# Kernel optimization log

Measured on AMD Instinct MI355X. Metric: run time of the kernel, lower is better.

## Reference

```python
import jax, jax.numpy as jnp
import numpy as np

IN, H, OUT = 128, 256, 128
B, T = 256, 512
EPS = 1e-5


def gru_cell(x, h, w_ih, w_hh, b_ih, b_hh):
    # PyTorch GRUCell: gates ordered (r, z, n)
    gi = x @ w_ih.T + b_ih            # (B, 3H)
    gh = h @ w_hh.T + b_hh            # (B, 3H)
    gi_r, gi_z, gi_n = jnp.split(gi, 3, axis=-1)
    gh_r, gh_z, gh_n = jnp.split(gh, 3, axis=-1)
    r = jax.nn.sigmoid(gi_r + gh_r)
    z = jax.nn.sigmoid(gi_z + gh_z)
    n = jnp.tanh(gi_n + r * gh_n)
    return (1.0 - z) * n + z * h


def setup_inputs() -> dict:
    key = jax.random.key(0)
    ks = jax.random.split(key, 12)
    s_in = 1.0 / np.sqrt(H)
    u = lambda k, shp: jax.random.uniform(k, shp, jnp.float32, -s_in, s_in)
    return {
        "x": jax.random.normal(ks[0], (B, T, IN), jnp.float32),
        "w_ih1": u(ks[1], (3 * H, IN)),
        "w_hh1": u(ks[2], (3 * H, H)),
        "b_ih1": u(ks[3], (3 * H,)),
        "b_hh1": u(ks[4], (3 * H,)),
        "w_ih2": u(ks[5], (3 * H, H)),
        "w_hh2": u(ks[6], (3 * H, H)),
        "b_ih2": u(ks[7], (3 * H,)),
        "b_hh2": u(ks[8], (3 * H,)),
        "gamma": jnp.ones((H,), jnp.float32),
        "beta": jnp.zeros((H,), jnp.float32),
        "fc_w": u(ks[9], (OUT, H)),
        "fc_b": u(ks[10], (OUT,)),
    }


def reference(x, w_ih1, w_hh1, b_ih1, b_hh1, w_ih2, w_hh2, b_ih2, b_hh2,
              gamma, beta, fc_w, fc_b):
    batch = x.shape[0]
    h0 = (jnp.zeros((batch, H), x.dtype), jnp.zeros((batch, H), x.dtype))

    def step(carry, xt):
        h1, h2 = carry
        h1 = gru_cell(xt, h1, w_ih1, w_hh1, b_ih1, b_hh1)
        h2 = gru_cell(h1, h2, w_ih2, w_hh2, b_ih2, b_hh2)
        return (h1, h2), h2

    _, seq_hidden = jax.lax.scan(step, h0, jnp.swapaxes(x, 0, 1))  # (T, B, H)
    seq_hidden = jnp.swapaxes(seq_hidden, 0, 1)                    # (B, T, H)

    # SyncBatchNorm in training mode: batch statistics over (batch*time)
    flat = seq_hidden.reshape(-1, H)
    mean = flat.mean(axis=0)
    var = flat.var(axis=0)  # biased variance, as used for normalization
    normed = (flat - mean) * jax.lax.rsqrt(var + EPS) * gamma + beta

    # Hardtanh(-2, 2), temporal mean, linear projection
    act = jnp.clip(normed, -2.0, 2.0).reshape(batch, -1, H)
    summary = act.mean(axis=1)                                     # (B, H)
    return summary @ fc_w.T + fc_b
```

## Files before the change

### kernel.cpp

```cpp
#include <hip/hip_runtime.h>
#include <stdint.h>

#define TT 512
#define BB 256
#define HH 256
#define II 128
#define OUTD 128
#define EPSV 1e-5f

#define NCL 32
#define RPC 8
#define RD1 32
#define RD2 16
#define HPAD 264
#define SPIN_CAP (1 << 17)

#define P_M1 0
#define P_A  1
#define P_M2 2
#define P_B  3

#define OFF_PROG     0u
#define OFF_BNSUM    1024u
#define OFF_BNSQ     2048u
#define OFF_ZERO_END 3072u
#define OFF_GI1      65536u
#define GI_SLOT      16384u
#define GI1_BYTES    ((unsigned)NCL*RD1*GI_SLOT)
#define OFF_H1R      (OFF_GI1 + GI1_BYTES)
#define H1R_BYTES    ((unsigned)NCL*RD2*4096u)
#define OFF_GI2      (OFF_H1R + H1R_BYTES)
#define GI2_BYTES    ((unsigned)NCL*RD2*GI_SLOT)
#define OFF_H2SEQ    (OFF_GI2 + GI2_BYTES)

typedef short bf16x8 __attribute__((ext_vector_type(8)));
typedef float f32x4  __attribute__((ext_vector_type(4)));
typedef unsigned long long u64;

__device__ __forceinline__ short f2bf(float v) {
    unsigned u = __float_as_uint(v);
    u += 0x7fffu + ((u >> 16) & 1u);
    return (short)(u >> 16);
}
__device__ __forceinline__ float bf2f(short s) {
    return __uint_as_float(((unsigned)(unsigned short)s) << 16);
}
__device__ __forceinline__ float bf2f_lo(unsigned u) {
    return __uint_as_float(u << 16);
}
__device__ __forceinline__ float bf2f_hi(unsigned u) {
    return __uint_as_float(u & 0xffff0000u);
}
__device__ __forceinline__ unsigned pk2bf(float a, float b) {
    return (unsigned)(unsigned short)f2bf(a) | ((unsigned)(unsigned short)f2bf(b) << 16);
}
__device__ __forceinline__ bf16x8 ldfrag_f32(const float* __restrict__ p) {
    const float4* q = (const float4*)p;
    float4 a = q[0], b = q[1];
    bf16x8 f;
    f[0]=f2bf(a.x); f[1]=f2bf(a.y); f[2]=f2bf(a.z); f[3]=f2bf(a.w);
    f[4]=f2bf(b.x); f[5]=f2bf(b.y); f[6]=f2bf(b.z); f[7]=f2bf(b.w);
    return f;
}
__device__ __forceinline__ float sigm_f(float x) {
    float e = __expf(-x);
    return __builtin_amdgcn_rcpf(1.f + e);
}
__device__ __forceinline__ float tanh_f(float x) {
    float ax = fabsf(x);
    float e  = __expf(-2.f * ax);
    float t  = (1.f - e) * __builtin_amdgcn_rcpf(1.f + e);
    return copysignf(t, x);
}
__device__ __forceinline__ void poll_ge(const unsigned* p, int tgt) {
    if (tgt <= 0) return;
    int spins = 0;
    while ((int)__hip_atomic_load((unsigned*)p, __ATOMIC_RELAXED, __HIP_MEMORY_SCOPE_SYSTEM) < tgt) {
        __builtin_amdgcn_s_sleep(2);
        if (++spins > SPIN_CAP) break;
    }
    asm volatile("" ::: "memory");
}
__device__ __forceinline__ void poll2_ge(const unsigned* p1, int t1, const unsigned* p2, int t2) {
    int spins = 0;
    for (;;) {
        int a = (int)__hip_atomic_load((unsigned*)p1, __ATOMIC_RELAXED, __HIP_MEMORY_SCOPE_SYSTEM);
        int b = (int)__hip_atomic_load((unsigned*)p2, __ATOMIC_RELAXED, __HIP_MEMORY_SCOPE_SYSTEM);
        if (a >= t1 && b >= t2) break;
        __builtin_amdgcn_s_sleep(2);
        if (++spins > SPIN_CAP) break;
    }
    asm volatile("" ::: "memory");
}
__device__ __forceinline__ void post_prog(unsigned* p, int v) {
    __hip_atomic_store(p, (unsigned)v, __ATOMIC_RELAXED, __HIP_MEMORY_SCOPE_SYSTEM);
}
__device__ __forceinline__ unsigned ld_u32_coh(const unsigned* p) {
    return __hip_atomic_load((unsigned*)p, __ATOMIC_RELAXED, __HIP_MEMORY_SCOPE_SYSTEM);
}
__device__ __forceinline__ void st_u32_coh(unsigned* p, unsigned v) {
    __hip_atomic_store(p, v, __ATOMIC_RELAXED, __HIP_MEMORY_SCOPE_SYSTEM);
}
__device__ __forceinline__ u64 ld_u64_coh(const u64* p) {
    return __hip_atomic_load((u64*)p, __ATOMIC_RELAXED, __HIP_MEMORY_SCOPE_SYSTEM);
}
__device__ __forceinline__ void st_u64_coh(u64* p, u64 v) {
    __hip_atomic_store(p, v, __ATOMIC_RELAXED, __HIP_MEMORY_SCOPE_SYSTEM);
}
#define CFENCE() asm volatile("" ::: "memory")

__global__ void __launch_bounds__(512, 1)
gru_pipe(const float* __restrict__ x,
         const float* __restrict__ wih1, const float* __restrict__ whh1,
         const float* __restrict__ bih1, const float* __restrict__ bhh1,
         const float* __restrict__ wih2, const float* __restrict__ whh2,
         const float* __restrict__ bih2, const float* __restrict__ bhh2,
         char* __restrict__ ws)
{
    const int tid = threadIdx.x, wave = tid >> 6, lane = tid & 63;
    const int qd = lane >> 4, ln = lane & 15;
    const int stage = blockIdx.x & 3;
    const int cl    = blockIdx.x >> 2;
    const int grow0 = cl * RPC;

    unsigned* prog = (unsigned*)(ws + OFF_PROG) + cl * 4;
    short* h2seq = (short*)(ws + OFF_H2SEQ);

    __shared__ __align__(16) short hb[2][16][HPAD];
    {
        short* z = &hb[0][0][0];
        for (int i = tid; i < 2*16*HPAD; i += 512) z[i] = 0;
    }
    __syncthreads();

    if (stage == 0) {
        bf16x8 Wi[2][3][4]; f32x4 cinit[2][3];
        #pragma unroll
        for (int b2 = 0; b2 < 2; ++b2)
        #pragma unroll
        for (int g = 0; g < 3; ++g) {
            const int grow = g*256 + (wave*2 + b2)*16 + ln;
            #pragma unroll
            for (int kc = 0; kc < 4; ++kc)
                Wi[b2][g][kc] = ldfrag_f32(wih1 + grow*II + kc*32 + qd*8);
            float c0 = bih1[grow] + (g < 2 ? bhh1[grow] : 0.f);
            cinit[b2][g] = f32x4{c0, c0, c0, c0};
        }
        const float* xr = x + (size_t)(grow0 + (ln>>2)*2 + (ln&1)) * (TT*II) + qd*8;
        float4 xp[8];
        #pragma unroll
        for (int kc = 0; kc < 4; ++kc) {
            xp[2*kc]   = *(const float4*)(xr + kc*32);
            xp[2*kc+1] = *(const float4*)(xr + kc*32 + 4);
        }

        for (int t = 0; t < TT; ++t) {
            if (tid == 0 && t >= 2) post_prog(&prog[P_M1], t);
            if ((t & 7) == 0) poll_ge(&prog[P_A], t - 24);
            CFENCE();
            bf16x8 a[4];
            #pragma unroll
            for (int kc = 0; kc < 4; ++kc) {
                float4 u = xp[2*kc], v = xp[2*kc+1];
                bf16x8 f;
                f[0]=f2bf(u.x); f[1]=f2bf(u.y); f[2]=f2bf(u.z); f[3]=f2bf(u.w);
                f[4]=f2bf(v.x); f[5]=f2bf(v.y); f[6]=f2bf(v.z); f[7]=f2bf(v.w);
                a[kc] = f;
            }
            if (t + 1 < TT) {
                const float* xn = xr + (size_t)(t+1)*II;
                #pragma unroll
                for (int kc = 0; kc < 4; ++kc) {
                    xp[2*kc]   = *(const float4*)(xn + kc*32);
                    xp[2*kc+1] = *(const float4*)(xn + kc*32 + 4);
                }
            }
            CFENCE();
            f32x4 acc[2][3];
            #pragma unroll
            for (int b2 = 0; b2 < 2; ++b2)
            #pragma unroll
            for (int g = 0; g < 3; ++g) acc[b2][g] = cinit[b2][g];
            #pragma unroll
            for (int kc = 0; kc < 4; ++kc)
            #pragma unroll
            for (int b2 = 0; b2 < 2; ++b2)
            #pragma unroll
            for (int g = 0; g < 3; ++g)
                acc[b2][g] = __builtin_amdgcn_mfma_f32_16x16x32_bf16(a[kc], Wi[b2][g][kc], acc[b2][g], 0, 0, 0);
            CFENCE();
            char* slot = ws + OFF_GI1 + ((size_t)cl*RD1 + (t & (RD1-1)))*GI_SLOT;
            unsigned* rz = (unsigned*)slot;
            u64* nn = (u64*)(slot + 8192);
            #pragma unroll
            for (int b2 = 0; b2 < 2; ++b2) {
                const int tile = wave*2 + b2;
                st_u32_coh(rz + (tile*2 + 0)*64 + lane, pk2bf(acc[b2][0][0], acc[b2][0][1]));
                st_u32_coh(rz + (tile*2 + 1)*64 + lane, pk2bf(acc[b2][1][0], acc[b2][1][1]));
                union { float f[2]; u64 u; } np;
                np.f[0] = acc[b2][2][0]; np.f[1] = acc[b2][2][1];
                st_u64_coh(nn + tile*64 + lane, np.u);
            }
            asm volatile("s_waitcnt vmcnt(14)" ::: "memory");
            __builtin_amdgcn_sched_barrier(0);
            __builtin_amdgcn_s_barrier();
        }
        __syncthreads();
        if (tid == 0) post_prog(&prog[P_M1], 1000000);

    } else if (stage == 1) {
        bf16x8 Wh[2][3][8]; float bnn[2];
        #pragma unroll
        for (int b2 = 0; b2 < 2; ++b2) {
            const int colg = (wave*2 + b2)*16 + ln;
            #pragma unroll
            for (int g = 0; g < 3; ++g)
                #pragma unroll
                for (int kc = 0; kc < 8; ++kc)
                    Wh[b2][g][kc] = ldfrag_f32(whh1 + (g*256 + colg)*HH + kc*32 + qd*8);
            bnn[b2] = bhh1[512 + colg];
        }
        float hold[2][2] = {{0.f,0.f},{0.f,0.f}};
        unsigned pr0, pr1, pz0, pz1; u64 pn0, pn1;
        const int tile0 = wave*2, tile1 = wave*2 + 1;

        poll_ge(&prog[P_M1], 2);
        {
            char* slot = ws + OFF_GI1 + (size_t)cl*RD1*GI_SLOT;
            const unsigned* rz = (const unsigned*)slot;
            const u64* nn = (const u64*)(slot + 8192);
            pr0 = ld_u32_coh(rz + (tile0*2+0)*64 + lane);
            pz0 = ld_u32_coh(rz + (tile0*2+1)*64 + lane);
            pn0 = ld_u64_coh(nn + tile0*64 + lane);
            pr1 = ld_u32_coh(rz + (tile1*2+0)*64 + lane);
            pz1 = ld_u32_coh(rz + (tile1*2+1)*64 + lane);
            pn1 = ld_u64_coh(nn + tile1*64 + lane);
        }

        for (int t = 0; t < TT; ++t) {
            if (tid == 0 && t >= 2) post_prog(&prog[P_A], t);
            if ((t & 7) == 0) poll2_ge(&prog[P_M1], t + 10, &prog[P_M2], t - 9);
            CFENCE();
            f32x4 aR[2], aZ[2], aN[2]; float gn[2][2];
            aR[0] = f32x4{bf2f_lo(pr0), bf2f_hi(pr0), 0.f, 0.f};
            aZ[0] = f32x4{bf2f_lo(pz0), bf2f_hi(pz0), 0.f, 0.f};
            aR[1] = f32x4{bf2f_lo(pr1), bf2f_hi(pr1), 0.f, 0.f};
            aZ[1] = f32x4{bf2f_lo(pz1), bf2f_hi(pz1), 0.f, 0.f};
            { union { u64 u; float f[2]; } c; c.u = pn0; gn[0][0]=c.f[0]; gn[0][1]=c.f[1];
              c.u = pn1; gn[1][0]=c.f[0]; gn[1][1]=c.f[1]; }
            aN[0] = f32x4{bnn[0], bnn[0], 0.f, 0.f};
            aN[1] = f32x4{bnn[1], bnn[1], 0.f, 0.f};
            if (t + 1 < TT) {
                char* slot = ws + OFF_GI1 + ((size_t)cl*RD1 + ((t+1) & (RD1-1)))*GI_SLOT;
                const unsigned* rz = (const unsigned*)slot;
                const u64* nn = (const u64*)(slot + 8192);
                pr0 = ld_u32_coh(rz + (tile0*2+0)*64 + lane);
                pz0 = ld_u32_coh(rz + (tile0*2+1)*64 + lane);
                pn0 = ld_u64_coh(nn + tile0*64 + lane);
                pr1 = ld_u32_coh(rz + (tile1*2+0)*64 + lane);
                pz1 = ld_u32_coh(rz + (tile1*2+1)*64 + lane);
                pn1 = ld_u64_coh(nn + tile1*64 + lane);
            }
            CFENCE();
            const int rb = (t + 1) & 1, wb = t & 1;
            #pragma unroll
            for (int kc = 0; kc < 8; ++kc) {
                bf16x8 f = *(const bf16x8*)&hb[rb][ln][kc*32 + qd*8];
                aR[0] = __builtin_amdgcn_mfma_f32_16x16x32_bf16(f, Wh[0][0][kc], aR[0], 0,0,0);
                aR[1] = __builtin_amdgcn_mfma_f32_16x16x32_bf16(f, Wh[1][0][kc], aR[1], 0,0,0);
                aZ[0] = __builtin_amdgcn_mfma_f32_16x16x32_bf16(f, Wh[0][1][kc], aZ[0], 0,0,0);
                aZ[1] = __builtin_amdgcn_mfma_f32_16x16x32_bf16(f, Wh[1][1][kc], aZ[1], 0,0,0);
                aN[0] = __builtin_amdgcn_mfma_f32_16x16x32_bf16(f, Wh[0][2][kc], aN[0], 0,0,0);
                aN[1] = __builtin_amdgcn_mfma_f32_16x16x32_bf16(f, Wh[1][2][kc], aN[1], 0,0,0);
            }
            CFENCE();
            unsigned* h1slot = (unsigned*)(ws + OFF_H1R + ((size_t)cl*RD2 + (t & (RD2-1)))*4096u);
            #pragma unroll
            for (int b2 = 0; b2 < 2; ++b2) {
                const int colg = (wave*2 + b2)*16 + ln;
                unsigned pk = 0;
                #pragma unroll
                for (int r = 0; r < 2; ++r) {
                    float rg = sigm_f(aR[b2][r]);
                    float zg = sigm_f(aZ[b2][r]);
                    float ng = tanh_f(gn[b2][r] + rg * aN[b2][r]);
                    float h  = (1.f - zg)*ng + zg*hold[b2][r];
                    hold[b2][r] = h;
                    short hs = f2bf(h);
                    hb[wb][qd*4 + r][colg] = hs;
                    pk |= (unsigned)(unsigned short)hs << (16*r);
                }
                st_u32_coh(h1slot + colg*4 + qd, pk);
            }
            asm volatile("s_waitcnt vmcnt(8) lgkmcnt(0)" ::: "memory");
            __builtin_amdgcn_sched_barrier(0);
            __builtin_amdgcn_s_barrier();
        }
        __syncthreads();
        if (tid == 0) post_prog(&prog[P_A], 1000000);

    } else if (stage == 2) {
        bf16x8 Wi[2][3][8]; float c0s[2][3];
        #pragma unroll
        for (int b2 = 0; b2 < 2; ++b2)
        #pragma unroll
        for (int g = 0; g < 3; ++g) {
            const int grow = g*256 + (wave*2 + b2)*16 + ln;
            #pragma unroll
            for (int kc = 0; kc < 8; ++kc)
                Wi[b2][g][kc] = ldfrag_f32(wih2 + grow*HH + kc*32 + qd*8);
            c0s[b2][g] = bih2[grow] + (g < 2 ? bhh2[grow] : 0.f);
        }
        const int base = (tid & 1) * 8, pcol = tid >> 1;
        u64 vcur;

        poll_ge(&prog[P_A], 2);
        {
            const u64* h1s = (const u64*)(ws + OFF_H1R + (size_t)cl*RD2*4096u);
            u64 v = ld_u64_coh(h1s + tid);
            unsigned lo = (unsigned)v, hi = (unsigned)(v >> 32);
            hb[0][base + 0][pcol] = (short)lo;
            hb[0][base + 1][pcol] = (short)(lo >> 16);
            hb[0][base + 4][pcol] = (short)hi;
            hb[0][base + 5][pcol] = (short)(hi >> 16);
        }
        poll_ge(&prog[P_A], 3);
        vcur = ld_u64_coh((const u64*)(ws + OFF_H1R + ((size_t)cl*RD2 + 1)*4096u) + tid);
        __syncthreads();

        for (int u = 0; u < TT; ++u) {
            if (tid == 0 && u >= 2) post_prog(&prog[P_M2], u);
            if ((u & 1) == 0) poll2_ge(&prog[P_A], u + 5, &prog[P_B], u - 13);
            CFENCE();
            if (u + 1 < TT) {
                unsigned lo = (unsigned)vcur, hi = (unsigned)(vcur >> 32);
                hb[(u+1) & 1][base + 0][pcol] = (short)lo;
                hb[(u+1) & 1][base + 1][pcol] = (short)(lo >> 16);
                hb[(u+1) & 1][base + 4][pcol] = (short)hi;
                hb[(u+1) & 1][base + 5][pcol] = (short)(hi >> 16);
            }
            if (u + 2 < TT)
                vcur = ld_u64_coh((const u64*)(ws + OFF_H1R + ((size_t)cl*RD2 + ((u+2) & (RD2-1)))*4096u) + tid);
            CFENCE();
            f32x4 acc[2][3];
            #pragma unroll
            for (int b2 = 0; b2 < 2; ++b2)
            #pragma unroll
            for (int g = 0; g < 3; ++g) {
                float c0 = c0s[b2][g];
                acc[b2][g] = f32x4{c0, c0, c0, c0};
            }
            #pragma unroll
            for (int kc = 0; kc < 8; ++kc) {
                bf16x8 f = *(const bf16x8*)&hb[u & 1][ln][kc*32 + qd*8];
                #pragma unroll
                for (int b2 = 0; b2 < 2; ++b2)
                #pragma unroll
                for (int g = 0; g < 3; ++g)
                    acc[b2][g] = __builtin_amdgcn_mfma_f32_16x16x32_bf16(f, Wi[b2][g][kc], acc[b2][g], 0, 0, 0);
            }
            CFENCE();
            char* slot = ws + OFF_GI2 + ((size_t)cl*RD2 + (u & (RD2-1)))*GI_SLOT;
            unsigned* rz = (unsigned*)slot;
            u64* nn = (u64*)(slot + 8192);
            #pragma unroll
            for (int b2 = 0; b2 < 2; ++b2) {
                const int tile = wave*2 + b2;
                st_u32_coh(rz + (tile*2 + 0)*64 + lane, pk2bf(acc[b2][0][0], acc[b2][0][1]));
                st_u32_coh(rz + (tile*2 + 1)*64 + lane, pk2bf(acc[b2][1][0], acc[b2][1][1]));
                union { float f[2]; u64 u; } np;
                np.f[0] = acc[b2][2][0]; np.f[1] = acc[b2][2][1];
                st_u64_coh(nn + tile*64 + lane, np.u);
            }
            asm volatile("s_waitcnt vmcnt(7) lgkmcnt(0)" ::: "memory");
            __builtin_amdgcn_sched_barrier(0);
            __builtin_amdgcn_s_barrier();
        }
        __syncthreads();
        if (tid == 0) post_prog(&prog[P_M2], 1000000);

    } else {
        bf16x8 Wh[2][3][8]; float bnn[2];
        #pragma unroll
        for (int b2 = 0; b2 < 2; ++b2) {
            const int colg = (wave*2 + b2)*16 + ln;
            #pragma unroll
            for (int g = 0; g < 3; ++g)
                #pragma unroll
                for (int kc = 0; kc < 8; ++kc)
                    Wh[b2][g][kc] = ldfrag_f32(whh2 + (g*256 + colg)*HH + kc*32 + qd*8);
            bnn[b2] = bhh2[512 + colg];
        }
        float* bnsum = (float*)(ws + OFF_BNSUM);
        float* bnsq  = (float*)(ws + OFF_BNSQ);
        float hold[2][2] = {{0.f,0.f},{0.f,0.f}};
        float cbs[2] = {0.f, 0.f}, cbq[2] = {0.f, 0.f};
        unsigned pr0, pr1, pz0, pz1; u64 pn0, pn1;
        const int tile0 = wave*2, tile1 = wave*2 + 1;

        poll_ge(&prog[P_M2], 2);
        {
            char* slot = ws + OFF_GI2 + (size_t)cl*RD2*GI_SLOT;
            const unsigned* rz = (const unsigned*)slot;
            const u64* nn = (const u64*)(slot + 8192);
            pr0 = ld_u32_coh(rz + (tile0*2+0)*64 + lane);
            pz0 = ld_u32_coh(rz + (tile0*2+1)*64 + lane);
            pn0 = ld_u64_coh(nn + tile0*64 + lane);
            pr1 = ld_u32_coh(rz + (tile1*2+0)*64 + lane);
            pz1 = ld_u32_coh(rz + (tile1*2+1)*64 + lane);
            pn1 = ld_u64_coh(nn + tile1*64 + lane);
        }
        __syncthreads();

        for (int v = 0; v < TT; ++v) {
            if (tid == 0 && v >= 2) post_prog(&prog[P_B], v);
            if ((v & 1) == 0) poll_ge(&prog[P_M2], v + 4);
            CFENCE();
            f32x4 aR[2], aZ[2], aN[2]; float gn[2][2];
            aR[0] = f32x4{bf2f_lo(pr0), bf2f_hi(pr0), 0.f, 0.f};
            aZ[0] = f32x4{bf2f_lo(pz0), bf2f_hi(pz0), 0.f, 0.f};
            aR[1] = f32x4{bf2f_lo(pr1), bf2f_hi(pr1), 0.f, 0.f};
            aZ[1] = f32x4{bf2f_lo(pz1), bf2f_hi(pz1), 0.f, 0.f};
            { union { u64 u; float f[2]; } c; c.u = pn0; gn[0][0]=c.f[0]; gn[0][1]=c.f[1];
              c.u = pn1; gn[1][0]=c.f[0]; gn[1][1]=c.f[1]; }
            aN[0] = f32x4{bnn[0], bnn[0], 0.f, 0.f};
            aN[1] = f32x4{bnn[1], bnn[1], 0.f, 0.f};
            if (v + 1 < TT) {
                char* slot = ws + OFF_GI2 + ((size_t)cl*RD2 + ((v+1) & (RD2-1)))*GI_SLOT;
                const unsigned* rz = (const unsigned*)slot;
                const u64* nn = (const u64*)(slot + 8192);
                pr0 = ld_u32_coh(rz + (tile0*2+0)*64 + lane);
                pz0 = ld_u32_coh(rz + (tile0*2+1)*64 + lane);
                pn0 = ld_u64_coh(nn + tile0*64 + lane);
                pr1 = ld_u32_coh(rz + (tile1*2+0)*64 + lane);
                pz1 = ld_u32_coh(rz + (tile1*2+1)*64 + lane);
                pn1 = ld_u64_coh(nn + tile1*64 + lane);
            }
            CFENCE();
            const int rb = (v + 1) & 1, wb = v & 1;
            #pragma unroll
            for (int kc = 0; kc < 8; ++kc) {
                bf16x8 f = *(const bf16x8*)&hb[rb][ln][kc*32 + qd*8];
                aR[0] = __builtin_amdgcn_mfma_f32_16x16x32_bf16(f, Wh[0][0][kc], aR[0], 0,0,0);
                aR[1] = __builtin_amdgcn_mfma_f32_16x16x32_bf16(f, Wh[1][0][kc], aR[1], 0,0,0);
                aZ[0] = __builtin_amdgcn_mfma_f32_16x16x32_bf16(f, Wh[0][1][kc], aZ[0], 0,0,0);
                aZ[1] = __builtin_amdgcn_mfma_f32_16x16x32_bf16(f, Wh[1][1][kc], aZ[1], 0,0,0);
                aN[0] = __builtin_amdgcn_mfma_f32_16x16x32_bf16(f, Wh[0][2][kc], aN[0], 0,0,0);
                aN[1] = __builtin_amdgcn_mfma_f32_16x16x32_bf16(f, Wh[1][2][kc], aN[1], 0,0,0);
            }
            CFENCE();
            #pragma unroll
            for (int b2 = 0; b2 < 2; ++b2) {
                const int colg = (wave*2 + b2)*16 + ln;
                #pragma unroll
                for (int r = 0; r < 2; ++r) {
                    float rg = sigm_f(aR[b2][r]);
                    float zg = sigm_f(aZ[b2][r]);
                    float ng = tanh_f(gn[b2][r] + rg * aN[b2][r]);
                    float h  = (1.f - zg)*ng + zg*hold[b2][r];
                    hold[b2][r] = h;
                    cbs[b2] += h; cbq[b2] += h*h;
                    short hs = f2bf(h);
                    hb[wb][qd*4 + r][colg] = hs;
                    h2seq[((size_t)v*BB + grow0 + qd*2 + r)*HH + colg] = hs;
                }
            }
            asm volatile("s_waitcnt vmcnt(10) lgkmcnt(0)" ::: "memory");
            __builtin_amdgcn_sched_barrier(0);
            __builtin_amdgcn_s_barrier();
        }
        #pragma unroll
        for (int b2 = 0; b2 < 2; ++b2) {
            const int colg = (wave*2 + b2)*16 + ln;
            atomicAdd(&bnsum[colg], cbs[b2]);
            atomicAdd(&bnsq[colg],  cbq[b2]);
        }
        __syncthreads();
        if (tid == 0) post_prog(&prog[P_B], 1000000);
    }
}

__global__ void gru_final(const char* __restrict__ ws,
                          const float* __restrict__ gamma, const float* __restrict__ beta,
                          const float* __restrict__ fcw, const float* __restrict__ fcb,
                          float* __restrict__ out)
{
    __shared__ float summ[HH];
    const int b = blockIdx.x, c = threadIdx.x;
    const float* bnsum = (const float*)(ws + OFF_BNSUM);
    const float* bnsq  = (const float*)(ws + OFF_BNSQ);
    const short* h2seq = (const short*)(ws + OFF_H2SEQ);

    const float inv = 1.f / (float)(BB * TT);
    float mean = bnsum[c] * inv;
    float var  = bnsq[c] * inv - mean * mean;
    float scale = rsqrtf(var + EPSV) * gamma[c];
    float shift = beta[c] - mean * scale;

    const short* p = h2seq + (size_t)b*HH + c;
    float acc = 0.f;
    #pragma unroll 4
    for (int t = 0; t < TT; ++t) {
        float v = bf2f(p[(size_t)t*BB*HH]) * scale + shift;
        v = fminf(fmaxf(v, -2.f), 2.f);
        acc += v;
    }
    summ[c] = acc * (1.f / TT);
    __syncthreads();
    if (c < OUTD) {
        float d = fcb[c];
        const float* wr = fcw + c*HH;
        #pragma unroll 8
        for (int h = 0; h < HH; ++h) d += wr[h] * summ[h];
        out[b*OUTD + c] = d;
    }
}

extern "C" void kernel_launch(void* const* d_in, const int* in_sizes, int n_in,
                              void* d_out, int out_size, void* d_ws, size_t ws_size,
                              hipStream_t stream)
{
    const float* x    = (const float*)d_in[0];
    const float* wih1 = (const float*)d_in[1];
    const float* whh1 = (const float*)d_in[2];
    const float* bih1 = (const float*)d_in[3];
    const float* bhh1 = (const float*)d_in[4];
    const float* wih2 = (const float*)d_in[5];
    const float* whh2 = (const float*)d_in[6];
    const float* bih2 = (const float*)d_in[7];
    const float* bhh2 = (const float*)d_in[8];
    const float* gamma= (const float*)d_in[9];
    const float* beta = (const float*)d_in[10];
    const float* fcw  = (const float*)d_in[11];
    const float* fcb  = (const float*)d_in[12];
    char* ws = (char*)d_ws;

    (void)hipMemsetAsync(ws, 0, OFF_ZERO_END, stream);

    hipLaunchKernelGGL(gru_pipe, dim3(NCL*4), dim3(512), 0, stream,
                       x, wih1, whh1, bih1, bhh1, wih2, whh2, bih2, bhh2, ws);

    hipLaunchKernelGGL(gru_final, dim3(BB), dim3(HH), 0, stream,
                       (const char*)ws, gamma, beta, fcw, fcb, (float*)d_out);
}
```

Baseline: 1.870 ms.

## Deepen cross-stage prefetch to two steps and halve progress-flag traffic

```diff
diff --git a/kernel.cpp b/kernel.cpp
--- a/kernel.cpp
+++ b/kernel.cpp
@@ -11,7 +11,7 @@
 #define NCL 32
 #define RPC 8
 #define RD1 32
-#define RD2 16
+#define RD2 32
 #define HPAD 264
 #define SPIN_CAP (1 << 17)
 
@@ -45,12 +45,8 @@
 __device__ __forceinline__ float bf2f(short s) {
     return __uint_as_float(((unsigned)(unsigned short)s) << 16);
 }
-__device__ __forceinline__ float bf2f_lo(unsigned u) {
-    return __uint_as_float(u << 16);
-}
-__device__ __forceinline__ float bf2f_hi(unsigned u) {
-    return __uint_as_float(u & 0xffff0000u);
-}
+__device__ __forceinline__ float bf2f_lo(unsigned u) { return __uint_as_float(u << 16); }
+__device__ __forceinline__ float bf2f_hi(unsigned u) { return __uint_as_float(u & 0xffff0000u); }
 __device__ __forceinline__ unsigned pk2bf(float a, float b) {
     return (unsigned)(unsigned short)f2bf(a) | ((unsigned)(unsigned short)f2bf(b) << 16);
 }
@@ -155,7 +151,6 @@
         }
 
         for (int t = 0; t < TT; ++t) {
-            if (tid == 0 && t >= 2) post_prog(&prog[P_M1], t);
             if ((t & 7) == 0) poll_ge(&prog[P_A], t - 24);
             CFENCE();
             bf16x8 a[4];
@@ -201,10 +196,15 @@
                 np.f[0] = acc[b2][2][0]; np.f[1] = acc[b2][2][1];
                 st_u64_coh(nn + tile*64 + lane, np.u);
             }
-            asm volatile("s_waitcnt vmcnt(14)" ::: "memory");
+            if (t & 1) {
+                asm volatile("s_waitcnt vmcnt(14)" ::: "memory");
+                if (tid == 0) post_prog(&prog[P_M1], t - 1);
+            }
+            asm volatile("s_waitcnt lgkmcnt(0)" ::: "memory");
             __builtin_amdgcn_sched_barrier(0);
             __builtin_amdgcn_s_barrier();
         }
+        asm volatile("s_waitcnt vmcnt(0)" ::: "memory");
         __syncthreads();
         if (tid == 0) post_prog(&prog[P_M1], 1000000);
 
@@ -221,81 +221,93 @@
             bnn[b2] = bhh1[512 + colg];
         }
         float hold[2][2] = {{0.f,0.f},{0.f,0.f}};
-        unsigned pr0, pr1, pz0, pz1; u64 pn0, pn1;
+        unsigned pr0[2], pz0[2], pr1[2], pz1[2]; u64 pn0[2], pn1[2];
         const int tile0 = wave*2, tile1 = wave*2 + 1;
 
         poll_ge(&prog[P_M1], 2);
-        {
-            char* slot = ws + OFF_GI1 + (size_t)cl*RD1*GI_SLOT;
+        #pragma unroll
+        for (int s = 0; s < 2; ++s) {
+            char* slot = ws + OFF_GI1 + ((size_t)cl*RD1 + s)*GI_SLOT;
             const unsigned* rz = (const unsigned*)slot;
             const u64* nn = (const u64*)(slot + 8192);
-            pr0 = ld_u32_coh(rz + (tile0*2+0)*64 + lane);
-            pz0 = ld_u32_coh(rz + (tile0*2+1)*64 + lane);
-            pn0 = ld_u64_coh(nn + tile0*64 + lane);
-            pr1 = ld_u32_coh(rz + (tile1*2+0)*64 + lane);
-            pz1 = ld_u32_coh(rz + (tile1*2+1)*64 + lane);
-            pn1 = ld_u64_coh(nn + tile1*64 + lane);
-        }
-
-        for (int t = 0; t < TT; ++t) {
-            if (tid == 0 && t >= 2) post_prog(&prog[P_A], t);
-            if ((t & 7) == 0) poll2_ge(&prog[P_M1], t + 10, &prog[P_M2], t - 9);
-            CFENCE();
-            f32x4 aR[2], aZ[2], aN[2]; float gn[2][2];
-            aR[0] = f32x4{bf2f_lo(pr0), bf2f_hi(pr0), 0.f, 0.f};
-            aZ[0] = f32x4{bf2f_lo(pz0), bf2f_hi(pz0), 0.f, 0.f};
-            aR[1] = f32x4{bf2f_lo(pr1), bf2f_hi(pr1), 0.f, 0.f};
-            aZ[1] = f32x4{bf2f_lo(pz1), bf2f_hi(pz1), 0.f, 0.f};
-            { union { u64 u; float f[2]; } c; c.u = pn0; gn[0][0]=c.f[0]; gn[0][1]=c.f[1];
-              c.u = pn1; gn[1][0]=c.f[0]; gn[1][1]=c.f[1]; }
-            aN[0] = f32x4{bnn[0], bnn[0], 0.f, 0.f};
-            aN[1] = f32x4{bnn[1], bnn[1], 0.f, 0.f};
-            if (t + 1 < TT) {
-                char* slot = ws + OFF_GI1 + ((size_t)cl*RD1 + ((t+1) & (RD1-1)))*GI_SLOT;
-                const unsigned* rz = (const unsigned*)slot;
-                const u64* nn = (const u64*)(slot + 8192);
-                pr0 = ld_u32_coh(rz + (tile0*2+0)*64 + lane);
-                pz0 = ld_u32_coh(rz + (tile0*2+1)*64 + lane);
-                pn0 = ld_u64_coh(nn + tile0*64 + lane);
-                pr1 = ld_u32_coh(rz + (tile1*2+0)*64 + lane);
-                pz1 = ld_u32_coh(rz + (tile1*2+1)*64 + lane);
-                pn1 = ld_u64_coh(nn + tile1*64 + lane);
-            }
-            CFENCE();
-            const int rb = (t + 1) & 1, wb = t & 1;
-            #pragma unroll
-            for (int kc = 0; kc < 8; ++kc) {
-                bf16x8 f = *(const bf16x8*)&hb[rb][ln][kc*32 + qd*8];
-                aR[0] = __builtin_amdgcn_mfma_f32_16x16x32_bf16(f, Wh[0][0][kc], aR[0], 0,0,0);
-                aR[1] = __builtin_amdgcn_mfma_f32_16x16x32_bf16(f, Wh[1][0][kc], aR[1], 0,0,0);
-                aZ[0] = __builtin_amdgcn_mfma_f32_16x16x32_bf16(f, Wh[0][1][kc], aZ[0], 0,0,0);
-                aZ[1] = __builtin_amdgcn_mfma_f32_16x16x32_bf16(f, Wh[1][1][kc], aZ[1], 0,0,0);
-                aN[0] = __builtin_amdgcn_mfma_f32_16x16x32_bf16(f, Wh[0][2][kc], aN[0], 0,0,0);
-                aN[1] = __builtin_amdgcn_mfma_f32_16x16x32_bf16(f, Wh[1][2][kc], aN[1], 0,0,0);
-            }
-            CFENCE();
-            unsigned* h1slot = (unsigned*)(ws + OFF_H1R + ((size_t)cl*RD2 + (t & (RD2-1)))*4096u);
-            #pragma unroll
-            for (int b2 = 0; b2 < 2; ++b2) {
-                const int colg = (wave*2 + b2)*16 + ln;
-                unsigned pk = 0;
-                #pragma unroll
-                for (int r = 0; r < 2; ++r) {
-                    float rg = sigm_f(aR[b2][r]);
-                    float zg = sigm_f(aZ[b2][r]);
-                    float ng = tanh_f(gn[b2][r] + rg * aN[b2][r]);
-                    float h  = (1.f - zg)*ng + zg*hold[b2][r];
-                    hold[b2][r] = h;
-                    short hs = f2bf(h);
-                    hb[wb][qd*4 + r][colg] = hs;
-                    pk |= (unsigned)(unsigned short)hs << (16*r);
-                }
-                st_u32_coh(h1slot + colg*4 + qd, pk);
-            }
-            asm volatile("s_waitcnt vmcnt(8) lgkmcnt(0)" ::: "memory");
-            __builtin_amdgcn_sched_barrier(0);
-            __builtin_amdgcn_s_barrier();
-        }
+            pr0[s] = ld_u32_coh(rz + (tile0*2+0)*64 + lane);
+            pz0[s] = ld_u32_coh(rz + (tile0*2+1)*64 + lane);
+            pn0[s] = ld_u64_coh(nn + tile0*64 + lane);
+            pr1[s] = ld_u32_coh(rz + (tile1*2+0)*64 + lane);
+            pz1[s] = ld_u32_coh(rz + (tile1*2+1)*64 + lane);
+            pn1[s] = ld_u64_coh(nn + tile1*64 + lane);
+        }
+
+#define A_STEP(T, P)                                                           \
+        {                                                                      \
+            if (((T) & 7) == 0) poll2_ge(&prog[P_M1], (T)+10, &prog[P_M2], (T)-24); \
+            CFENCE();                                                          \
+            f32x4 aR[2], aZ[2], aN[2]; float gn[2][2];                         \
+            aR[0] = f32x4{bf2f_lo(pr0[P]), bf2f_hi(pr0[P]), 0.f, 0.f};         \
+            aZ[0] = f32x4{bf2f_lo(pz0[P]), bf2f_hi(pz0[P]), 0.f, 0.f};         \
+            aR[1] = f32x4{bf2f_lo(pr1[P]), bf2f_hi(pr1[P]), 0.f, 0.f};         \
+            aZ[1] = f32x4{bf2f_lo(pz1[P]), bf2f_hi(pz1[P]), 0.f, 0.f};         \
+            { union { u64 u; float f[2]; } c;                                  \
+              c.u = pn0[P]; gn[0][0]=c.f[0]; gn[0][1]=c.f[1];                  \
+              c.u = pn1[P]; gn[1][0]=c.f[0]; gn[1][1]=c.f[1]; }                \
+            aN[0] = f32x4{bnn[0], bnn[0], 0.f, 0.f};                           \
+            aN[1] = f32x4{bnn[1], bnn[1], 0.f, 0.f};                           \
+            if ((T) + 2 < TT) {                 \
+                char* slot = ws + OFF_GI1 + ((size_t)cl*RD1 + (((T)+2) & (RD1-1)))*GI_SLOT; \
+                const unsigned* rz = (const unsigned*)slot;                    \
+                const u64* nn = (const u64*)(slot + 8192);                     \
+                pr0[P] = ld_u32_coh(rz + (tile0*2+0)*64 + lane);               \
+                pz0[P] = ld_u32_coh(rz + (tile0*2+1)*64 + lane);               \
+                pn0[P] = ld_u64_coh(nn + tile0*64 + lane);                     \
+                pr1[P] = ld_u32_coh(rz + (tile1*2+0)*64 + lane);               \
+                pz1[P] = ld_u32_coh(rz + (tile1*2+1)*64 + lane);               \
+                pn1[P] = ld_u64_coh(nn + tile1*64 + lane);                     \
+            }                                                                  \
+            CFENCE();                                                          \
+            const int rb = ((T) + 1) & 1, wb = (T) & 1;                        \
+            _Pragma("unroll")                                                  \
+            for (int kc = 0; kc < 8; ++kc) {                                   \
+                bf16x8 f = *(const bf16x8*)&hb[rb][ln][kc*32 + qd*8];          \
+                aR[0] = __builtin_amdgcn_mfma_f32_16x16x32_bf16(f, Wh[0][0][kc], aR[0], 0,0,0); \
+                aR[1] = __builtin_amdgcn_mfma_f32_16x16x32_bf16(f, Wh[1][0][kc], aR[1], 0,0,0); \
+                aZ[0] = __builtin_amdgcn_mfma_f32_16x16x32_bf16(f, Wh[0][1][kc], aZ[0], 0,0,0); \
+                aZ[1] = __builtin_amdgcn_mfma_f32_16x16x32_bf16(f, Wh[1][1][kc], aZ[1], 0,0,0); \
+                aN[0] = __builtin_amdgcn_mfma_f32_16x16x32_bf16(f, Wh[0][2][kc], aN[0], 0,0,0); \
+                aN[1] = __builtin_amdgcn_mfma_f32_16x16x32_bf16(f, Wh[1][2][kc], aN[1], 0,0,0); \
+            }                                                                  \
+            CFENCE();                                                          \
+            unsigned* h1slot = (unsigned*)(ws + OFF_H1R + ((size_t)cl*RD2 + ((T) & (RD2-1)))*4096u); \
+            _Pragma("unroll")                                                  \
+            for (int b2 = 0; b2 < 2; ++b2) {                                   \
+                const int colg = (wave*2 + b2)*16 + ln;                        \
+                unsigned pk = 0;                                               \
+                _Pragma("unroll")                                              \
+                for (int r = 0; r < 2; ++r) {                                  \
+                    float rg = sigm_f(aR[b2][r]);                              \
+                    float zg = sigm_f(aZ[b2][r]);                              \
+                    float ng = tanh_f(gn[b2][r] + rg * aN[b2][r]);             \
+                    float h  = (1.f - zg)*ng + zg*hold[b2][r];                 \
+                    hold[b2][r] = h;                                           \
+                    short hs = f2bf(h);                                        \
+                    hb[wb][qd*4 + r][colg] = hs;                               \
+                    pk |= (unsigned)(unsigned short)hs << (16*r);              \
+                }                                                              \
+                st_u32_coh(h1slot + colg*4 + qd, pk);                          \
+            }                                                                  \
+            if ((T) & 1) {                                                     \
+                asm volatile("s_waitcnt vmcnt(8)" ::: "memory");               \
+                if (tid == 0) post_prog(&prog[P_A], (T) - 1);                  \
+            }                                                                  \
+            asm volatile("s_waitcnt lgkmcnt(0)" ::: "memory");                 \
+            __builtin_amdgcn_sched_barrier(0);                                 \
+            __builtin_amdgcn_s_barrier();                                      \
+        }
+        for (int t = 0; t < TT; t += 2) {
+            A_STEP(t,   0);
+            A_STEP(t+1, 1);
+        }
+#undef A_STEP
+        asm volatile("s_waitcnt vmcnt(0)" ::: "memory");
         __syncthreads();
         if (tid == 0) post_prog(&prog[P_A], 1000000);
 
@@ -312,7 +324,7 @@
             c0s[b2][g] = bih2[grow] + (g < 2 ? bhh2[grow] : 0.f);
         }
         const int base = (tid & 1) * 8, pcol = tid >> 1;
-        u64 vcur;
+        u64 vc[2];
 
         poll_ge(&prog[P_A], 2);
         {
@@ -324,58 +336,68 @@
             hb[0][base + 4][pcol] = (short)hi;
             hb[0][base + 5][pcol] = (short)(hi >> 16);
         }
-        poll_ge(&prog[P_A], 3);
-        vcur = ld_u64_coh((const u64*)(ws + OFF_H1R + ((size_t)cl*RD2 + 1)*4096u) + tid);
+        vc[0] = ld_u64_coh((const u64*)(ws + OFF_H1R + ((size_t)cl*RD2 + 1)*4096u) + tid);
+        vc[1] = ld_u64_coh((const u64*)(ws + OFF_H1R + ((size_t)cl*RD2 + 2)*4096u) + tid);
         __syncthreads();
 
-        for (int u = 0; u < TT; ++u) {
-            if (tid == 0 && u >= 2) post_prog(&prog[P_M2], u);
-            if ((u & 1) == 0) poll2_ge(&prog[P_A], u + 5, &prog[P_B], u - 13);
-            CFENCE();
-            if (u + 1 < TT) {
-                unsigned lo = (unsigned)vcur, hi = (unsigned)(vcur >> 32);
-                hb[(u+1) & 1][base + 0][pcol] = (short)lo;
-                hb[(u+1) & 1][base + 1][pcol] = (short)(lo >> 16);
-                hb[(u+1) & 1][base + 4][pcol] = (short)hi;
-                hb[(u+1) & 1][base + 5][pcol] = (short)(hi >> 16);
-            }
-            if (u + 2 < TT)
-                vcur = ld_u64_coh((const u64*)(ws + OFF_H1R + ((size_t)cl*RD2 + ((u+2) & (RD2-1)))*4096u) + tid);
-            CFENCE();
-            f32x4 acc[2][3];
-            #pragma unroll
-            for (int b2 = 0; b2 < 2; ++b2)
-            #pragma unroll
-            for (int g = 0; g < 3; ++g) {
-                float c0 = c0s[b2][g];
-                acc[b2][g] = f32x4{c0, c0, c0, c0};
-            }
-            #pragma unroll
-            for (int kc = 0; kc < 8; ++kc) {
-                bf16x8 f = *(const bf16x8*)&hb[u & 1][ln][kc*32 + qd*8];
-                #pragma unroll
-                for (int b2 = 0; b2 < 2; ++b2)
-                #pragma unroll
-                for (int g = 0; g < 3; ++g)
-                    acc[b2][g] = __builtin_amdgcn_mfma_f32_16x16x32_bf16(f, Wi[b2][g][kc], acc[b2][g], 0, 0, 0);
-            }
-            CFENCE();
-            char* slot = ws + OFF_GI2 + ((size_t)cl*RD2 + (u & (RD2-1)))*GI_SLOT;
-            unsigned* rz = (unsigned*)slot;
-            u64* nn = (u64*)(slot + 8192);
-            #pragma unroll
-            for (int b2 = 0; b2 < 2; ++b2) {
-                const int tile = wave*2 + b2;
-                st_u32_coh(rz + (tile*2 + 0)*64 + lane, pk2bf(acc[b2][0][0], acc[b2][0][1]));
-                st_u32_coh(rz + (tile*2 + 1)*64 + lane, pk2bf(acc[b2][1][0], acc[b2][1][1]));
-                union { float f[2]; u64 u; } np;
-                np.f[0] = acc[b2][2][0]; np.f[1] = acc[b2][2][1];
-                st_u64_coh(nn + tile*64 + lane, np.u);
-            }
-            asm volatile("s_waitcnt vmcnt(7) lgkmcnt(0)" ::: "memory");
-            __builtin_amdgcn_sched_barrier(0);
-            __builtin_amdgcn_s_barrier();
-        }
+#define M2_STEP(U, P)                                                          \
+        {                                                                      \
+            if (((U) & 7) == 0) poll2_ge(&prog[P_A], (U)+11, &prog[P_B], (U)-24); \
+            CFENCE();                                                          \
+            if ((U) + 1 < TT) {        \
+                unsigned lo = (unsigned)vc[P], hi = (unsigned)(vc[P] >> 32);   \
+                hb[((U)+1) & 1][base + 0][pcol] = (short)lo;                   \
+                hb[((U)+1) & 1][base + 1][pcol] = (short)(lo >> 16);           \
+                hb[((U)+1) & 1][base + 4][pcol] = (short)hi;                   \
+                hb[((U)+1) & 1][base + 5][pcol] = (short)(hi >> 16);           \
+            }                                                                  \
+            if ((U) + 3 < TT)                                                  \
+                vc[P] = ld_u64_coh((const u64*)(ws + OFF_H1R + ((size_t)cl*RD2 + (((U)+3) & (RD2-1)))*4096u) + tid); \
+            CFENCE();                                                          \
+            f32x4 acc[2][3];                                                   \
+            _Pragma("unroll")                                                  \
+            for (int b2 = 0; b2 < 2; ++b2)                                     \
+            _Pragma("unroll")                                                  \
+            for (int g = 0; g < 3; ++g) {                                      \
+                float c0 = c0s[b2][g];                                         \
+                acc[b2][g] = f32x4{c0, c0, c0, c0};                            \
+            }                                                                  \
+            _Pragma("unroll")                                                  \
+            for (int kc = 0; kc < 8; ++kc) {                                   \
+                bf16x8 f = *(const bf16x8*)&hb[(U) & 1][ln][kc*32 + qd*8];     \
+                _Pragma("unroll")                                              \
+                for (int b2 = 0; b2 < 2; ++b2)                                 \
+                _Pragma("unroll")                                              \
+                for (int g = 0; g < 3; ++g)                                    \
+                    acc[b2][g] = __builtin_amdgcn_mfma_f32_16x16x32_bf16(f, Wi[b2][g][kc], acc[b2][g], 0, 0, 0); \
+            }                                                                  \
+            CFENCE();                                                          \
+            char* slot = ws + OFF_GI2 + ((size_t)cl*RD2 + ((U) & (RD2-1)))*GI_SLOT; \
+            unsigned* rz = (unsigned*)slot;                                    \
+            u64* nn = (u64*)(slot + 8192);                                     \
+            _Pragma("unroll")                                                  \
+            for (int b2 = 0; b2 < 2; ++b2) {                                   \
+                const int tile = wave*2 + b2;                                  \
+                st_u32_coh(rz + (tile*2 + 0)*64 + lane, pk2bf(acc[b2][0][0], acc[b2][0][1])); \
+                st_u32_coh(rz + (tile*2 + 1)*64 + lane, pk2bf(acc[b2][1][0], acc[b2][1][1])); \
+                union { float f[2]; u64 u; } np;                               \
+                np.f[0] = acc[b2][2][0]; np.f[1] = acc[b2][2][1];              \
+                st_u64_coh(nn + tile*64 + lane, np.u);                         \
+            }                                                                  \
+            if ((U) & 1) {                                                     \
+                asm volatile("s_waitcnt vmcnt(7)" ::: "memory");               \
+                if (tid == 0) post_prog(&prog[P_M2], (U) - 1);                 \
+            }                                                                  \
+            asm volatile("s_waitcnt lgkmcnt(0)" ::: "memory");                 \
+            __builtin_amdgcn_sched_barrier(0);                                 \
+            __builtin_amdgcn_s_barrier();                                      \
+        }
+        for (int u = 0; u < TT; u += 2) {
+            M2_STEP(u,   0);
+            M2_STEP(u+1, 1);
+        }
+#undef M2_STEP
+        asm volatile("s_waitcnt vmcnt(0)" ::: "memory");
         __syncthreads();
         if (tid == 0) post_prog(&prog[P_M2], 1000000);
 
@@ -395,80 +417,88 @@
         float* bnsq  = (float*)(ws + OFF_BNSQ);
         float hold[2][2] = {{0.f,0.f},{0.f,0.f}};
         float cbs[2] = {0.f, 0.f}, cbq[2] = {0.f, 0.f};
-        unsigned pr0, pr1, pz0, pz1; u64 pn0, pn1;
+        unsigned pr0[2], pz0[2], pr1[2], pz1[2]; u64 pn0[2], pn1[2];
         const int tile0 = wave*2, tile1 = wave*2 + 1;
 
         poll_ge(&prog[P_M2], 2);
-        {
-            char* slot = ws + OFF_GI2 + (size_t)cl*RD2*GI_SLOT;
+        #pragma unroll
+        for (int s = 0; s < 2; ++s) {
+            char* slot = ws + OFF_GI2 + ((size_t)cl*RD2 + s)*GI_SLOT;
             const unsigned* rz = (const unsigned*)slot;
             const u64* nn = (const u64*)(slot + 8192);
-            pr0 = ld_u32_coh(rz + (tile0*2+0)*64 + lane);
-            pz0 = ld_u32_coh(rz + (tile0*2+1)*64 + lane);
-            pn0 = ld_u64_coh(nn + tile0*64 + lane);
-            pr1 = ld_u32_coh(rz + (tile1*2+0)*64 + lane);
-            pz1 = ld_u32_coh(rz + (tile1*2+1)*64 + lane);
-            pn1 = ld_u64_coh(nn + tile1*64 + lane);
+            pr0[s] = ld_u32_coh(rz + (tile0*2+0)*64 + lane);
+            pz0[s] = ld_u32_coh(rz + (tile0*2+1)*64 + lane);
+            pn0[s] = ld_u64_coh(nn + tile0*64 + lane);
+            pr1[s] = ld_u32_coh(rz + (tile1*2+0)*64 + lane);
+            pz1[s] = ld_u32_coh(rz + (tile1*2+1)*64 + lane);
+            pn1[s] = ld_u64_coh(nn + tile1*64 + lane);
         }
         __syncthreads();
 
-        for (int v = 0; v < TT; ++v) {
-            if (tid == 0 && v >= 2) post_prog(&prog[P_B], v);
-            if ((v & 1) == 0) poll_ge(&prog[P_M2], v + 4);
-            CFENCE();
-            f32x4 aR[2], aZ[2], aN[2]; float gn[2][2];
-            aR[0] = f32x4{bf2f_lo(pr0), bf2f_hi(pr0), 0.f, 0.f};
-            aZ[0] = f32x4{bf2f_lo(pz0), bf2f_hi(pz0), 0.f, 0.f};
-            aR[1] = f32x4{bf2f_lo(pr1), bf2f_hi(pr1), 0.f, 0.f};
-            aZ[1] = f32x4{bf2f_lo(pz1), bf2f_hi(pz1), 0.f, 0.f};
-            { union { u64 u; float f[2]; } c; c.u = pn0; gn[0][0]=c.f[0]; gn[0][1]=c.f[1];
-              c.u = pn1; gn[1][0]=c.f[0]; gn[1][1]=c.f[1]; }
-            aN[0] = f32x4{bnn[0], bnn[0], 0.f, 0.f};
-            aN[1] = f32x4{bnn[1], bnn[1], 0.f, 0.f};
-            if (v + 1 < TT) {
-                char* slot = ws + OFF_GI2 + ((size_t)cl*RD2 + ((v+1) & (RD2-1)))*GI_SLOT;
-                const unsigned* rz = (const unsigned*)slot;
-                const u64* nn = (const u64*)(slot + 8192);
-                pr0 = ld_u32_coh(rz + (tile0*2+0)*64 + lane);
-                pz0 = ld_u32_coh(rz + (tile0*2+1)*64 + lane);
-                pn0 = ld_u64_coh(nn + tile0*64 + lane);
-                pr1 = ld_u32_coh(rz + (tile1*2+0)*64 + lane);
-                pz1 = ld_u32_coh(rz + (tile1*2+1)*64 + lane);
-                pn1 = ld_u64_coh(nn + tile1*64 + lane);
-            }
-            CFENCE();
-            const int rb = (v + 1) & 1, wb = v & 1;
-            #pragma unroll
-            for (int kc = 0; kc < 8; ++kc) {
-                bf16x8 f = *(const bf16x8*)&hb[rb][ln][kc*32 + qd*8];
-                aR[0] = __builtin_amdgcn_mfma_f32_16x16x32_bf16(f, Wh[0][0][kc], aR[0], 0,0,0);
-                aR[1] = __builtin_amdgcn_mfma_f32_16x16x32_bf16(f, Wh[1][0][kc], aR[1], 0,0,0);
-                aZ[0] = __builtin_amdgcn_mfma_f32_16x16x32_bf16(f, Wh[0][1][kc], aZ[0], 0,0,0);
-                aZ[1] = __builtin_amdgcn_mfma_f32_16x16x32_bf16(f, Wh[1][1][kc], aZ[1], 0,0,0);
-                aN[0] = __builtin_amdgcn_mfma_f32_16x16x32_bf16(f, Wh[0][2][kc], aN[0], 0,0,0);
-                aN[1] = __builtin_amdgcn_mfma_f32_16x16x32_bf16(f, Wh[1][2][kc], aN[1], 0,0,0);
-            }
-            CFENCE();
-            #pragma unroll
-            for (int b2 = 0; b2 < 2; ++b2) {
-                const int colg = (wave*2 + b2)*16 + ln;
-                #pragma unroll
-                for (int r = 0; r < 2; ++r) {
-                    float rg = sigm_f(aR[b2][r]);
-                    float zg = sigm_f(aZ[b2][r]);
-                    float ng = tanh_f(gn[b2][r] + rg * aN[b2][r]);
-                    float h  = (1.f - zg)*ng + zg*hold[b2][r];
-                    hold[b2][r] = h;
-                    cbs[b2] += h; cbq[b2] += h*h;
-                    short hs = f2bf(h);
-                    hb[wb][qd*4 + r][colg] = hs;
-                    h2seq[((size_t)v*BB + grow0 + qd*2 + r)*HH + colg] = hs;
-                }
-            }
-            asm volatile("s_waitcnt vmcnt(10) lgkmcnt(0)" ::: "memory");
-            __builtin_amdgcn_sched_barrier(0);
-            __builtin_amdgcn_s_barrier();
-        }
+#define B_STEP(V, P)                                                           \
+        {                                                                      \
+            if (((V) & 7) == 0) poll_ge(&prog[P_M2], (V)+10);                  \
+            CFENCE();                                                          \
+            f32x4 aR[2], aZ[2], aN[2]; float gn[2][2];                         \
+            aR[0] = f32x4{bf2f_lo(pr0[P]), bf2f_hi(pr0[P]), 0.f, 0.f};         \
+            aZ[0] = f32x4{bf2f_lo(pz0[P]), bf2f_hi(pz0[P]), 0.f, 0.f};         \
+            aR[1] = f32x4{bf2f_lo(pr1[P]), bf2f_hi(pr1[P]), 0.f, 0.f};         \
+            aZ[1] = f32x4{bf2f_lo(pz1[P]), bf2f_hi(pz1[P]), 0.f, 0.f};         \
+            { union { u64 u; float f[2]; } c;                                  \
+              c.u = pn0[P]; gn[0][0]=c.f[0]; gn[0][1]=c.f[1];                  \
+              c.u = pn1[P]; gn[1][0]=c.f[0]; gn[1][1]=c.f[1]; }                \
+            aN[0] = f32x4{bnn[0], bnn[0], 0.f, 0.f};                           \
+            aN[1] = f32x4{bnn[1], bnn[1], 0.f, 0.f};                           \
+            if ((V) + 2 < TT) {                 \
+                char* slot = ws + OFF_GI2 + ((size_t)cl*RD2 + (((V)+2) & (RD2-1)))*GI_SLOT; \
+                const unsigned* rz = (const unsigned*)slot;                    \
+                const u64* nn = (const u64*)(slot + 8192);                     \
+                pr0[P] = ld_u32_coh(rz + (tile0*2+0)*64 + lane);               \
+                pz0[P] = ld_u32_coh(rz + (tile0*2+1)*64 + lane);               \
+                pn0[P] = ld_u64_coh(nn + tile0*64 + lane);                     \
+                pr1[P] = ld_u32_coh(rz + (tile1*2+0)*64 + lane);               \
+                pz1[P] = ld_u32_coh(rz + (tile1*2+1)*64 + lane);               \
+                pn1[P] = ld_u64_coh(nn + tile1*64 + lane);                     \
+            }                                                                  \
+            CFENCE();                                                          \
+            const int rb = ((V) + 1) & 1, wb = (V) & 1;                        \
+            _Pragma("unroll")                                                  \
+            for (int kc = 0; kc < 8; ++kc) {                                   \
+                bf16x8 f = *(const bf16x8*)&hb[rb][ln][kc*32 + qd*8];          \
+                aR[0] = __builtin_amdgcn_mfma_f32_16x16x32_bf16(f, Wh[0][0][kc], aR[0], 0,0,0); \
+                aR[1] = __builtin_amdgcn_mfma_f32_16x16x32_bf16(f, Wh[1][0][kc], aR[1], 0,0,0); \
+                aZ[0] = __builtin_amdgcn_mfma_f32_16x16x32_bf16(f, Wh[0][1][kc], aZ[0], 0,0,0); \
+                aZ[1] = __builtin_amdgcn_mfma_f32_16x16x32_bf16(f, Wh[1][1][kc], aZ[1], 0,0,0); \
+                aN[0] = __builtin_amdgcn_mfma_f32_16x16x32_bf16(f, Wh[0][2][kc], aN[0], 0,0,0); \
+                aN[1] = __builtin_amdgcn_mfma_f32_16x16x32_bf16(f, Wh[1][2][kc], aN[1], 0,0,0); \
+            }                                                                  \
+            CFENCE();                                                          \
+            _Pragma("unroll")                                                  \
+            for (int b2 = 0; b2 < 2; ++b2) {                                   \
+                const int colg = (wave*2 + b2)*16 + ln;                        \
+                _Pragma("unroll")                                              \
+                for (int r = 0; r < 2; ++r) {                                  \
+                    float rg = sigm_f(aR[b2][r]);                              \
+                    float zg = sigm_f(aZ[b2][r]);                              \
+                    float ng = tanh_f(gn[b2][r] + rg * aN[b2][r]);             \
+                    float h  = (1.f - zg)*ng + zg*hold[b2][r];                 \
+                    hold[b2][r] = h;                                           \
+                    cbs[b2] += h; cbq[b2] += h*h;                              \
+                    short hs = f2bf(h);                                        \
+                    hb[wb][qd*4 + r][colg] = hs;                               \
+                    h2seq[((size_t)(V)*BB + grow0 + qd*2 + r)*HH + colg] = hs; \
+                }                                                              \
+            }                                                                  \
+            if (((V) & 1) && tid == 0) post_prog(&prog[P_B], (V) - 1);         \
+            asm volatile("s_waitcnt lgkmcnt(0)" ::: "memory");                 \
+            __builtin_amdgcn_sched_barrier(0);                                 \
+            __builtin_amdgcn_s_barrier();                                      \
+        }
+        for (int v = 0; v < TT; v += 2) {
+            B_STEP(v,   0);
+            B_STEP(v+1, 1);
+        }
+#undef B_STEP
         #pragma unroll
         for (int b2 = 0; b2 < 2; ++b2) {
             const int colg = (wave*2 + b2)*16 + ln;
```

New measurement: 2.006 ms. +7.3%, slower.
